# Kernel optimization log

Measured on AMD Instinct MI355X. Metric: run time of the kernel, lower is better.

## Reference

```python
import jax, jax.numpy as jnp
import numpy as np

NUM_EXPERTS = 8
TOP_K = 2
HIDDEN = 768
INTERMEDIATE = 3072
NUM_TOKENS = 8192


def setup_inputs() -> dict:
    key = jax.random.key(0)
    k0, k1, k2, k3 = jax.random.split(key, 4)
    hidden_states = jax.random.normal(k0, (NUM_TOKENS, HIDDEN), dtype=jnp.float32)
    router_weight = jax.random.normal(k1, (NUM_EXPERTS, HIDDEN), dtype=jnp.float32) * 0.02
    w1 = jax.random.normal(k2, (NUM_EXPERTS, INTERMEDIATE, HIDDEN), dtype=jnp.float32) * 0.02
    w2 = jax.random.normal(k3, (NUM_EXPERTS, HIDDEN, INTERMEDIATE), dtype=jnp.float32) * 0.02
    bias = jnp.zeros((HIDDEN,), dtype=jnp.float32)
    return {"hidden_states": hidden_states, "router_weight": router_weight,
            "w1": w1, "w2": w2, "bias": bias}


def _moe_forward(hidden_states, router_weight, w1, w2, bias):
    T, H = hidden_states.shape
    E = w1.shape[0]
    # Router: ReplicatedLinear(H, E, bias=False)
    logits = hidden_states @ router_weight.T                      # [T, E]
    # fused_topk: softmax over all experts, then top-k, renormalize=False
    probs = jax.nn.softmax(logits, axis=-1)                       # [T, E]
    topk_w, topk_ids = jax.lax.top_k(probs, TOP_K)                # [T, K]
    # per-token per-expert combine weight (top-k ids are distinct)
    gates = jnp.sum(jax.nn.one_hot(topk_ids, E, dtype=probs.dtype) * topk_w[..., None], axis=1)  # [T, E]
    # Expert MLP: y_e = gelu(x @ w1[e].T) @ w2[e].T  (non-gated, activation_without_mul('gelu'))
    out = jnp.zeros_like(hidden_states)
    for e in range(E):  # small fixed expert count
        h = jax.nn.gelu(hidden_states @ w1[e].T, approximate=False)  # [T, I]
        out = out + gates[:, e:e + 1] * (h @ w2[e].T)                # [T, H]
    return out + bias


def reference(hidden_states, router_weight, w1, w2, bias):
    return _moe_forward(hidden_states, router_weight, w1, w2, bias)
```

## Files before the change

kernel.cpp:

```cpp
#include <hip/hip_runtime.h>
#include <hip/hip_bf16.h>
#include <math.h>

#define NT 8192
#define HD 768
#define ID 3072
#define NE 8
#define BK 32
#define MAXB 72
#define ASZ (256 * BK)
#define BSZ (128 * BK)
#define TSZ (256 * BK)
#define RT_BLOCKS 256
#define CW1_BLOCKS (NE * ID * HD / 4 / 1024)
#define G1_GEMM (MAXB * (ID / 128))
#define CW2_BLOCKS (NE * HD * ID / 4 / 2048)

typedef __bf16 bf16x8 __attribute__((ext_vector_type(8)));
typedef float f32x4 __attribute__((ext_vector_type(4)));

__device__ __forceinline__ unsigned short f2bf(float f) {
    union { float f; unsigned u; } v; v.f = f;
    unsigned r = v.u + 0x7FFFu + ((v.u >> 16) & 1u);
    return (unsigned short)(r >> 16);
}
__device__ __forceinline__ float bf2f(unsigned short b) {
    union { unsigned u; float f; } v; v.u = ((unsigned)b) << 16;
    return v.f;
}
__device__ __forceinline__ unsigned cvt_pk_bf16(float lo, float hi) {
    unsigned r;
    asm("v_cvt_pk_bf16_f32 %0, %1, %2" : "=v"(r) : "v"(lo), "v"(hi));
    return r;
}
__device__ __forceinline__ float gelu_s(float v) {
    float z = v * (1.5957691216057308f + 0.07135481283687945f * v * v);
    float e = __expf(-z);
    return v * __builtin_amdgcn_rcpf(1.0f + e);
}

__device__ __forceinline__ void gload16(const void* g, void* l) {
    auto* lds = reinterpret_cast<__attribute__((address_space(3))) unsigned int*>(
        reinterpret_cast<uintptr_t>(l));
    auto* gp = reinterpret_cast<const __attribute__((address_space(1))) unsigned int*>(
        reinterpret_cast<uintptr_t>(g));
    __builtin_amdgcn_global_load_lds(gp, lds, 16, 0, 0);
}

__device__ __forceinline__ void decode_em(const int* counts, int bsw, int& e, int& m0) {
    e = -1; m0 = 0;
    int s = 0;
#pragma unroll
    for (int q = 0; q < NE; q++) {
        int nb = (counts[q] + 255) >> 8;
        if (bsw >= s && bsw < s + nb) { e = q; m0 = (bsw - s) << 8; }
        s += nb;
    }
}

__global__ void k_front(const float* __restrict__ x, const float* __restrict__ rw,
                        const float4* __restrict__ w1, ushort4* __restrict__ w1b,
                        ushort4* __restrict__ xb4, float* __restrict__ gates,
                        uchar2* __restrict__ choice) {
    __shared__ float rws[NE * HD];
    const int tid = threadIdx.x;
    if (blockIdx.x >= RT_BLOCKS) {
        int base = (blockIdx.x - RT_BLOCKS) * 1024 + tid;
#pragma unroll
        for (int i = 0; i < 4; i++) {
            int idx = base + i * 256;
            float4 a = w1[idx];
            ushort4 ra;
            ra.x = f2bf(a.x); ra.y = f2bf(a.y); ra.z = f2bf(a.z); ra.w = f2bf(a.w);
            w1b[idx] = ra;
        }
        return;
    }
    for (int i = tid; i < NE * HD / 4; i += 256)
        ((float4*)rws)[i] = ((const float4*)rw)[i];
    __syncthreads();
    const int wid = tid >> 6, lane = tid & 63;
    const float4* rws4 = (const float4*)rws;
    for (int it = 0; it < 8; ++it) {
        const int t = blockIdx.x * 32 + wid * 8 + it;
        const float4* xp4 = (const float4*)(x + (size_t)t * HD);
        float acc[NE];
#pragma unroll
        for (int e = 0; e < NE; e++) acc[e] = 0.f;
#pragma unroll
        for (int j = 0; j < HD / 256; j++) {
            float4 v = xp4[lane + 64 * j];
            ushort4 o;
            o.x = f2bf(v.x); o.y = f2bf(v.y); o.z = f2bf(v.z); o.w = f2bf(v.w);
            xb4[(size_t)t * (HD / 4) + lane + 64 * j] = o;
#pragma unroll
            for (int e = 0; e < NE; e++) {
                float4 w = rws4[e * (HD / 4) + lane + 64 * j];
                acc[e] += v.x * w.x + v.y * w.y + v.z * w.z + v.w * w.w;
            }
        }
#pragma unroll
        for (int e = 0; e < NE; e++)
            for (int off = 32; off; off >>= 1) acc[e] += __shfl_xor(acc[e], off);
        if (lane == 0) {
            float mx = acc[0];
#pragma unroll
            for (int e = 1; e < NE; e++) mx = fmaxf(mx, acc[e]);
            float p[NE], s = 0.f;
#pragma unroll
            for (int e = 0; e < NE; e++) { p[e] = __expf(acc[e] - mx); s += p[e]; }
            float inv = 1.f / s;
            int i1 = 0; float b1 = p[0];
#pragma unroll
            for (int e = 1; e < NE; e++) if (p[e] > b1) { b1 = p[e]; i1 = e; }
            int i2 = (i1 == 0) ? 1 : 0; float b2 = p[i2];
#pragma unroll
            for (int e = 0; e < NE; e++) if (e != i1 && p[e] > b2) { b2 = p[e]; i2 = e; }
            choice[t].x = (unsigned char)i1;
            choice[t].y = (unsigned char)i2;
            gates[2 * t] = b1 * inv;
            gates[2 * t + 1] = b2 * inv;
        }
    }
}

__global__ void k_cnt(const uchar2* __restrict__ choice, int* __restrict__ ccnt) {
    const int e = blockIdx.x >> 3, c = blockIdx.x & 7;
    const int tid = threadIdx.x, wid = tid >> 6, lane = tid & 63;
    __shared__ int ws[4];
    int tot = 0;
#pragma unroll
    for (int p = 0; p < 4; p++) {
        int t = c * 1024 + p * 256 + tid;
        uchar2 ch = choice[t];
        bool m = (ch.x == e) || (ch.y == e);
        unsigned long long mask = __ballot(m);
        if (lane == 0) tot += __popcll(mask);
    }
    if (lane == 0) ws[wid] = tot;
    __syncthreads();
    if (tid == 0) ccnt[blockIdx.x] = ws[0] + ws[1] + ws[2] + ws[3];
}

__global__ void k_wr(const uchar2* __restrict__ choice, const int* __restrict__ ccnt,
                     int* __restrict__ lists, int* __restrict__ counts) {
    const int e = blockIdx.x >> 3, c = blockIdx.x & 7;
    const int tid = threadIdx.x, wid = tid >> 6, lane = tid & 63;
    __shared__ int wtot[4];
    __shared__ int running;
    if (tid == 0) {
        int b = 0;
        for (int q = 0; q < c; q++) b += ccnt[e * 8 + q];
        running = b;
        if (c == 7) counts[e] = b + ccnt[e * 8 + 7];
    }
    __syncthreads();
#pragma unroll
    for (int p = 0; p < 4; p++) {
        int t = c * 1024 + p * 256 + tid;
        uchar2 ch = choice[t];
        bool m1 = (ch.x == e), m2 = (ch.y == e);
        bool m = m1 || m2;
        int slot = m1 ? 2 * t : 2 * t + 1;
        unsigned long long mask = __ballot(m);
        int off = __popcll(mask & ((1ULL << lane) - 1ULL));
        if (lane == 0) wtot[wid] = __popcll(mask);
        __syncthreads();
        int base = running;
        for (int w = 0; w < wid; w++) base += wtot[w];
        if (m) lists[e * NT + base + off] = slot;
        __syncthreads();
        if (tid == 0) running += wtot[0] + wtot[1] + wtot[2] + wtot[3];
        __syncthreads();
    }
}

__launch_bounds__(512, 2)
__global__ void k_gemm1(const unsigned short* __restrict__ xb, const unsigned short* __restrict__ w1b,
                        const float4* __restrict__ w2, ushort4* __restrict__ w2b,
                        const int* __restrict__ lists, const int* __restrict__ counts,
                        unsigned short* __restrict__ hbuf) {
    const int tid = threadIdx.x;
    if (blockIdx.x >= G1_GEMM) {
        int base = (blockIdx.x - G1_GEMM) * 2048 + tid;
#pragma unroll
        for (int i = 0; i < 4; i++) {
            int idx = base + i * 512;
            float4 a = w2[idx];
            ushort4 ra;
            ra.x = f2bf(a.x); ra.y = f2bf(a.y); ra.z = f2bf(a.z); ra.w = f2bf(a.w);
            w2b[idx] = ra;
        }
        return;
    }
    const int mi = blockIdx.x % MAXB;
    const int ny = blockIdx.x / MAXB;
    const int bsw = (mi & 7) * (MAXB >> 3) + (mi >> 3);
    int e, m0;
    decode_em(counts, bsw, e, m0);
    if (e < 0) return;
    const int cnt = counts[e];
    const int n0 = ny * 128;
    __shared__ __align__(16) unsigned short As[3 * ASZ];
    __shared__ __align__(16) unsigned short Bs[3 * BSZ];
    __shared__ int slot_s[256];
    const int lane = tid & 63, wid = tid >> 6;
    if (tid < 256) {
        int r = m0 + tid;
        slot_s[tid] = lists[e * NT + (r < cnt ? r : cnt - 1)];
    }
    __syncthreads();

    const int rsub = lane >> 2;
    const int sw = (((lane & 3) ^ ((rsub >> 1) & 3)) * 8);
    const int row0 = wid * 16 + rsub;
    const unsigned short* gA0 = xb + (size_t)(slot_s[row0] >> 1) * HD + sw;
    const unsigned short* gA1 = xb + (size_t)(slot_s[row0 + 128] >> 1) * HD + sw;
    const unsigned short* gB0 = w1b + ((size_t)e * ID + n0 + row0) * HD + sw;
    auto stage = [&](int bf) {
        gload16(gA0, As + bf * ASZ + wid * 512);       gA0 += BK;
        gload16(gA1, As + bf * ASZ + (wid + 8) * 512); gA1 += BK;
        gload16(gB0, Bs + bf * BSZ + wid * 512);       gB0 += BK;
    };

    const int wr = wid >> 1, wc = wid & 1;
    const int l15 = lane & 15, l4 = lane >> 4;
    const int aBase = (wr * 64 + l15) * BK;
    const int bBase = (wc * 64 + l15) * BK;
    const int cs = (l4 ^ ((l15 >> 1) & 3)) * 8;

    f32x4 acc[4][4];
    f32x4 zero = {0.f, 0.f, 0.f, 0.f};
#pragma unroll
    for (int m = 0; m < 4; m++)
#pragma unroll
        for (int n = 0; n < 4; n++) acc[m][n] = zero;

    const int NK = HD / BK;
    stage(0); stage(1);
    int cur = 0, pf = 2;
    for (int kt = 0; kt < NK; ++kt) {
        if (kt + 1 < NK) asm volatile("s_waitcnt vmcnt(3)\ns_barrier" ::: "memory");
        else             asm volatile("s_waitcnt vmcnt(0)\ns_barrier" ::: "memory");
        if (kt + 2 < NK) { stage(pf); pf = (pf == 2) ? 0 : pf + 1; }
        const unsigned short* Ab = As + cur * ASZ;
        const unsigned short* Bb = Bs + cur * BSZ;
        bf16x8 a[4], b[4];
#pragma unroll
        for (int m = 0; m < 4; m++) a[m] = *(const bf16x8*)(Ab + aBase + m * 512 + cs);
#pragma unroll
        for (int n = 0; n < 4; n++) b[n] = *(const bf16x8*)(Bb + bBase + n * 512 + cs);
        __builtin_amdgcn_s_setprio(1);
#pragma unroll
        for (int m = 0; m < 4; m++)
#pragma unroll
            for (int n = 0; n < 4; n++)
                acc[m][n] = __builtin_amdgcn_mfma_f32_16x16x32_bf16(b[n], a[m], acc[m][n], 0, 0, 0);
        __builtin_amdgcn_s_setprio(0);
        cur = (cur == 2) ? 0 : cur + 1;
    }
    const int rj = l4 * 4;
#pragma unroll
    for (int m = 0; m < 4; m++) {
        int lr2 = wr * 64 + m * 16 + l15;
        if (m0 + lr2 < cnt) {
            int slot = slot_s[lr2];
            unsigned short* hp = hbuf + (size_t)slot * ID + n0 + wc * 64 + rj;
#pragma unroll
            for (int n = 0; n < 4; n++) {
                uint2 pk;
                pk.x = cvt_pk_bf16(gelu_s(acc[m][n][0]), gelu_s(acc[m][n][1]));
                pk.y = cvt_pk_bf16(gelu_s(acc[m][n][2]), gelu_s(acc[m][n][3]));
                *(uint2*)(hp + n * 16) = pk;
            }
        }
    }
}

__launch_bounds__(512, 2)
__global__ void k_gemm2(const unsigned short* __restrict__ hbuf, const unsigned short* __restrict__ w2b,
                        const int* __restrict__ lists, const int* __restrict__ counts,
                        const float* __restrict__ gates, unsigned short* __restrict__ pout) {
    const int bsw = (blockIdx.x & 7) * (MAXB >> 3) + (blockIdx.x >> 3);
    int e, m0;
    decode_em(counts, bsw, e, m0);
    if (e < 0) return;
    const int cnt = counts[e];
    const int n0 = blockIdx.y * 256;
    __shared__ __align__(16) unsigned short As[4 * TSZ];
    __shared__ __align__(16) unsigned short Bs[4 * TSZ];
    __shared__ int slot_s[256];
    const int tid = threadIdx.x, lane = tid & 63, wid = tid >> 6;
    if (tid < 256) {
        int r = m0 + tid;
        slot_s[tid] = lists[e * NT + (r < cnt ? r : cnt - 1)];
    }
    __syncthreads();

    const int rsub = lane >> 2;
    const int sw = (((lane & 3) ^ ((rsub >> 1) & 3)) * 8);
    const int row0 = wid * 16 + rsub;
    const unsigned short* gA0 = hbuf + (size_t)slot_s[row0] * ID + sw;
    const unsigned short* gA1 = hbuf + (size_t)slot_s[row0 + 128] * ID + sw;
    const unsigned short* gB0 = w2b + ((size_t)e * HD + n0 + row0) * ID + sw;
    const unsigned short* gB1 = w2b + ((size_t)e * HD + n0 + row0 + 128) * ID + sw;
    auto stageA = [&](int bf) {
        gload16(gA0, As + bf * TSZ + wid * 512);       gA0 += BK;
        gload16(gA1, As + bf * TSZ + (wid + 8) * 512); gA1 += BK;
    };
    auto stageB = [&](int bf) {
        gload16(gB0, Bs + bf * TSZ + wid * 512);       gB0 += BK;
        gload16(gB1, Bs + bf * TSZ + (wid + 8) * 512); gB1 += BK;
    };

    const int wr = wid >> 2, wc = wid & 3;
    const int l15 = lane & 15, l4 = lane >> 4;
    const int aBase = (wr * 128 + l15) * BK;
    const int bBase = (wc * 64 + l15) * BK;
    const int cs = (l4 ^ ((l15 >> 1) & 3)) * 8;

    f32x4 acc[8][4];
    f32x4 zero = {0.f, 0.f, 0.f, 0.f};
#pragma unroll
    for (int m = 0; m < 8; m++)
#pragma unroll
        for (int n = 0; n < 4; n++) acc[m][n] = zero;

    const int NK = ID / BK;
    stageA(0); stageB(0); stageA(1); stageB(1);
    asm volatile("s_waitcnt vmcnt(4)\ns_barrier" ::: "memory");
    for (int st = 0; st < NK; ++st) {
        const unsigned short* Ab = As + (st & 3) * TSZ;
        const unsigned short* Bb = Bs + (st & 3) * TSZ;
        bf16x8 b[4], a[4];
#pragma unroll
        for (int n = 0; n < 4; n++) b[n] = *(const bf16x8*)(Bb + bBase + n * 512 + cs);
#pragma unroll
        for (int m = 0; m < 4; m++) a[m] = *(const bf16x8*)(Ab + aBase + m * 512 + cs);
        if (st + 2 < NK) stageA((st + 2) & 3);
        __builtin_amdgcn_s_setprio(1);
#pragma unroll
        for (int m = 0; m < 4; m++)
#pragma unroll
            for (int n = 0; n < 4; n++)
                acc[m][n] = __builtin_amdgcn_mfma_f32_16x16x32_bf16(b[n], a[m], acc[m][n], 0, 0, 0);
        __builtin_amdgcn_s_setprio(0);
        asm volatile("s_barrier" ::: "memory");
        bf16x8 a2[4];
#pragma unroll
        for (int m = 0; m < 4; m++) a2[m] = *(const bf16x8*)(Ab + aBase + (m + 4) * 512 + cs);
        if (st + 2 < NK) stageB((st + 2) & 3);
        __builtin_amdgcn_s_setprio(1);
#pragma unroll
        for (int m = 0; m < 4; m++)
#pragma unroll
            for (int n = 0; n < 4; n++)
                acc[m + 4][n] = __builtin_amdgcn_mfma_f32_16x16x32_bf16(b[n], a2[m], acc[m + 4][n], 0, 0, 0);
        __builtin_amdgcn_s_setprio(0);
        if (st + 2 < NK) asm volatile("s_waitcnt vmcnt(4)\ns_barrier" ::: "memory");
        else             asm volatile("s_waitcnt vmcnt(0)\ns_barrier" ::: "memory");
    }
    const int rj = l4 * 4;
#pragma unroll
    for (int m = 0; m < 8; m++) {
        int lr2 = wr * 128 + m * 16 + l15;
        if (m0 + lr2 < cnt) {
            int slot = slot_s[lr2];
            float g = gates[slot];
            unsigned short* pp = pout + (size_t)slot * HD + n0 + wc * 64 + rj;
#pragma unroll
            for (int n = 0; n < 4; n++) {
                uint2 pk;
                pk.x = cvt_pk_bf16(g * acc[m][n][0], g * acc[m][n][1]);
                pk.y = cvt_pk_bf16(g * acc[m][n][2], g * acc[m][n][3]);
                *(uint2*)(pp + n * 16) = pk;
            }
        }
    }
}

__global__ void k_combine(const unsigned short* __restrict__ pout, const float* __restrict__ bias,
                          float4* __restrict__ out) {
    int idx = blockIdx.x * 256 + threadIdx.x;
    int t = idx / (HD / 4);
    int c = idx - t * (HD / 4);
    ushort4 a = ((const ushort4*)pout)[(size_t)t * (2 * HD / 4) + c];
    ushort4 b = ((const ushort4*)pout)[(size_t)t * (2 * HD / 4) + HD / 4 + c];
    float4 bb = ((const float4*)bias)[c];
    float4 r;
    r.x = bf2f(a.x) + bf2f(b.x) + bb.x;
    r.y = bf2f(a.y) + bf2f(b.y) + bb.y;
    r.z = bf2f(a.z) + bf2f(b.z) + bb.z;
    r.w = bf2f(a.w) + bf2f(b.w) + bb.w;
    out[idx] = r;
}

extern "C" void kernel_launch(void* const* d_in, const int* in_sizes, int n_in,
                              void* d_out, int out_size, void* d_ws, size_t ws_size,
                              hipStream_t stream) {
    const float* x    = (const float*)d_in[0];
    const float* rw   = (const float*)d_in[1];
    const float* w1   = (const float*)d_in[2];
    const float* w2   = (const float*)d_in[3];
    const float* bias = (const float*)d_in[4];
    float* out = (float*)d_out;

    char* ws = (char*)d_ws;
    size_t off = 0;
    auto alloc = [&](size_t bytes) -> char* {
        char* p = ws + off;
        off += (bytes + 255) & ~(size_t)255;
        return p;
    };
    int*            counts = (int*)alloc(NE * 4);
    int*            ccnt   = (int*)alloc(NE * 8 * 4);
    int*            lists  = (int*)alloc((size_t)NE * NT * 4);
    float*          gates  = (float*)alloc((size_t)NT * 2 * 4);
    uchar2*         choice = (uchar2*)alloc((size_t)NT * 2);
    unsigned short* xb     = (unsigned short*)alloc((size_t)NT * HD * 2);
    unsigned short* w1b    = (unsigned short*)alloc((size_t)NE * ID * HD * 2);
    unsigned short* w2b    = (unsigned short*)alloc((size_t)NE * HD * ID * 2);
    unsigned short* hbuf   = (unsigned short*)alloc((size_t)NT * 2 * ID * 2);
    unsigned short* pout   = (unsigned short*)alloc((size_t)NT * 2 * HD * 2);

    k_front<<<dim3(RT_BLOCKS + CW1_BLOCKS), dim3(256), 0, stream>>>(
        x, rw, (const float4*)w1, (ushort4*)w1b, (ushort4*)xb, gates, choice);
    k_cnt<<<dim3(64), dim3(256), 0, stream>>>(choice, ccnt);
    k_wr<<<dim3(64), dim3(256), 0, stream>>>(choice, ccnt, lists, counts);
    k_gemm1<<<dim3(G1_GEMM + CW2_BLOCKS), dim3(512), 0, stream>>>(
        xb, w1b, (const float4*)w2, (ushort4*)w2b, lists, counts, hbuf);
    k_gemm2<<<dim3(MAXB, HD / 256), dim3(512), 0, stream>>>(hbuf, w2b, lists, counts, gates, pout);
    k_combine<<<dim3(NT * HD / 4 / 256), dim3(256), 0, stream>>>(pout, bias, (float4*)out);
}
```

Before: 257.2 us.

## Enlarge gemm1 tile to 256x256 with split A/B staging pipeline

The first expert GEMM now computes a 256x256 output tile per block instead of 256x128, with each wave owning 128x64 (32 accumulators). Shared buffers become a 4-deep ring for both A and B, and loads of the A and B halves are interleaved between two MFMA phases with barriers in between. The aim is more reuse of each loaded tile, fewer blocks, and better overlap of global loads with compute. The cost is higher register pressure, 64 KB+ of LDS that may cut occupancy below the launch bound, and fewer blocks to balance across CUs.

```diff
diff --git a/kernel.cpp b/kernel.cpp
--- a/kernel.cpp
+++ b/kernel.cpp
@@ -8,12 +8,10 @@
 #define NE 8
 #define BK 32
 #define MAXB 72
-#define ASZ (256 * BK)
-#define BSZ (128 * BK)
 #define TSZ (256 * BK)
 #define RT_BLOCKS 256
 #define CW1_BLOCKS (NE * ID * HD / 4 / 1024)
-#define G1_GEMM (MAXB * (ID / 128))
+#define G1_GEMM (MAXB * (ID / 256))
 #define CW2_BLOCKS (NE * HD * ID / 4 / 2048)
 
 typedef __bf16 bf16x8 __attribute__((ext_vector_type(8)));
@@ -175,6 +173,7 @@
     }
 }
 
+
 __launch_bounds__(512, 2)
 __global__ void k_gemm1(const unsigned short* __restrict__ xb, const unsigned short* __restrict__ w1b,
                         const float4* __restrict__ w2, ushort4* __restrict__ w2b,
@@ -200,9 +199,9 @@
     decode_em(counts, bsw, e, m0);
     if (e < 0) return;
     const int cnt = counts[e];
-    const int n0 = ny * 128;
-    __shared__ __align__(16) unsigned short As[3 * ASZ];
-    __shared__ __align__(16) unsigned short Bs[3 * BSZ];
+    const int n0 = ny * 256;
+    __shared__ __align__(16) unsigned short As[4 * TSZ];
+    __shared__ __align__(16) unsigned short Bs[4 * TSZ];
     __shared__ int slot_s[256];
     const int lane = tid & 63, wid = tid >> 6;
     if (tid < 256) {
@@ -217,39 +216,41 @@
     const unsigned short* gA0 = xb + (size_t)(slot_s[row0] >> 1) * HD + sw;
     const unsigned short* gA1 = xb + (size_t)(slot_s[row0 + 128] >> 1) * HD + sw;
     const unsigned short* gB0 = w1b + ((size_t)e * ID + n0 + row0) * HD + sw;
-    auto stage = [&](int bf) {
-        gload16(gA0, As + bf * ASZ + wid * 512);       gA0 += BK;
-        gload16(gA1, As + bf * ASZ + (wid + 8) * 512); gA1 += BK;
-        gload16(gB0, Bs + bf * BSZ + wid * 512);       gB0 += BK;
+    const unsigned short* gB1 = w1b + ((size_t)e * ID + n0 + row0 + 128) * HD + sw;
+    auto stageA = [&](int bf) {
+        gload16(gA0, As + bf * TSZ + wid * 512);       gA0 += BK;
+        gload16(gA1, As + bf * TSZ + (wid + 8) * 512); gA1 += BK;
     };
-
-    const int wr = wid >> 1, wc = wid & 1;
+    auto stageB = [&](int bf) {
+        gload16(gB0, Bs + bf * TSZ + wid * 512);       gB0 += BK;
+        gload16(gB1, Bs + bf * TSZ + (wid + 8) * 512); gB1 += BK;
+    };
+
+    const int wr = wid >> 2, wc = wid & 3;
     const int l15 = lane & 15, l4 = lane >> 4;
-    const int aBase = (wr * 64 + l15) * BK;
+    const int aBase = (wr * 128 + l15) * BK;
     const int bBase = (wc * 64 + l15) * BK;
     const int cs = (l4 ^ ((l15 >> 1) & 3)) * 8;
 
-    f32x4 acc[4][4];
+    f32x4 acc[8][4];
     f32x4 zero = {0.f, 0.f, 0.f, 0.f};
 #pragma unroll
-    for (int m = 0; m < 4; m++)
+    for (int m = 0; m < 8; m++)
 #pragma unroll
         for (int n = 0; n < 4; n++) acc[m][n] = zero;
 
     const int NK = HD / BK;
-    stage(0); stage(1);
-    int cur = 0, pf = 2;
-    for (int kt = 0; kt < NK; ++kt) {
-        if (kt + 1 < NK) asm volatile("s_waitcnt vmcnt(3)\ns_barrier" ::: "memory");
-        else             asm volatile("s_waitcnt vmcnt(0)\ns_barrier" ::: "memory");
-        if (kt + 2 < NK) { stage(pf); pf = (pf == 2) ? 0 : pf + 1; }
-        const unsigned short* Ab = As + cur * ASZ;
-        const unsigned short* Bb = Bs + cur * BSZ;
-        bf16x8 a[4], b[4];
+    stageA(0); stageB(0); stageA(1); stageB(1);
+    asm volatile("s_waitcnt vmcnt(4)\ns_barrier" ::: "memory");
+    for (int st = 0; st < NK; ++st) {
+        const unsigned short* Ab = As + (st & 3) * TSZ;
+        const unsigned short* Bb = Bs + (st & 3) * TSZ;
+        bf16x8 b[4], a[4];
+#pragma unroll
+        for (int n = 0; n < 4; n++) b[n] = *(const bf16x8*)(Bb + bBase + n * 512 + cs);
 #pragma unroll
         for (int m = 0; m < 4; m++) a[m] = *(const bf16x8*)(Ab + aBase + m * 512 + cs);
-#pragma unroll
-        for (int n = 0; n < 4; n++) b[n] = *(const bf16x8*)(Bb + bBase + n * 512 + cs);
+        if (st + 2 < NK) stageA((st + 2) & 3);
         __builtin_amdgcn_s_setprio(1);
 #pragma unroll
         for (int m = 0; m < 4; m++)
@@ -257,12 +258,25 @@
             for (int n = 0; n < 4; n++)
                 acc[m][n] = __builtin_amdgcn_mfma_f32_16x16x32_bf16(b[n], a[m], acc[m][n], 0, 0, 0);
         __builtin_amdgcn_s_setprio(0);
-        cur = (cur == 2) ? 0 : cur + 1;
+        asm volatile("s_barrier" ::: "memory");
+        bf16x8 a2[4];
+#pragma unroll
+        for (int m = 0; m < 4; m++) a2[m] = *(const bf16x8*)(Ab + aBase + (m + 4) * 512 + cs);
+        if (st + 2 < NK) stageB((st + 2) & 3);
+        __builtin_amdgcn_s_setprio(1);
+#pragma unroll
+        for (int m = 0; m < 4; m++)
+#pragma unroll
+            for (int n = 0; n < 4; n++)
+                acc[m + 4][n] = __builtin_amdgcn_mfma_f32_16x16x32_bf16(b[n], a2[m], acc[m + 4][n], 0, 0, 0);
+        __builtin_amdgcn_s_setprio(0);
+        if (st + 2 < NK) asm volatile("s_waitcnt vmcnt(4)\ns_barrier" ::: "memory");
+        else             asm volatile("s_waitcnt vmcnt(0)\ns_barrier" ::: "memory");
     }
     const int rj = l4 * 4;
 #pragma unroll
-    for (int m = 0; m < 4; m++) {
-        int lr2 = wr * 64 + m * 16 + l15;
+    for (int m = 0; m < 8; m++) {
+        int lr2 = wr * 128 + m * 16 + l15;
         if (m0 + lr2 < cnt) {
             int slot = slot_s[lr2];
             unsigned short* hp = hbuf + (size_t)slot * ID + n0 + wc * 64 + rj;
```

Result: no change. 254.1 us (-1.2%).
